# Kernel tuning notes

Measured on AMD Instinct MI355X. Metric: run time of the kernel, lower is better.

The kernel has to match this reference:

```python
import jax, jax.numpy as jnp
import numpy as np

B, S, C = 4, 4096, 1024   # batch, input_size (seq len), channels
H, D, DK = 16, 64, 256    # nhead, head dim, dim_k (Linformer projection)


def setup_inputs() -> dict:
    key = jax.random.key(0)
    ks = jax.random.split(key, 9)
    s_in = 1.0 / np.sqrt(C)
    s_e = 1.0 / np.sqrt(S)
    return {
        'x':   jax.random.normal(ks[0], (B, S, C), jnp.float32),
        # per-head Q/K/V projection weights (Linear(channels, dim, bias=False))
        'Wq':  jax.random.normal(ks[1], (H, D, C), jnp.float32) * s_in,
        'Wk':  jax.random.normal(ks[2], (H, D, C), jnp.float32) * s_in,
        'Wv':  jax.random.normal(ks[3], (H, D, C), jnp.float32) * s_in,
        # shared (layerwise) E/F Linear(input_size, dim_k) with bias
        'E_w': jax.random.normal(ks[4], (DK, S), jnp.float32) * s_e,
        'E_b': jnp.zeros((DK,), jnp.float32),
        'F_w': jax.random.normal(ks[5], (DK, S), jnp.float32) * s_e,
        'F_b': jnp.zeros((DK,), jnp.float32),
        # output projection Linear(dim*nhead, channels)
        'Wo':  jax.random.normal(ks[6], (C, H * D), jnp.float32) * (1.0 / np.sqrt(H * D)),
        'bo':  jnp.zeros((C,), jnp.float32),
    }


def reference(x, Wq, Wk, Wv, E_w, E_b, F_w, F_b, Wo, bo):
    b, s, c = x.shape
    h, d, _ = Wq.shape
    # per-head projections (vectorized over the Python head loop)
    Q = jnp.einsum('bsc,hdc->bhsd', x, Wq)            # [B,H,S,D]
    Kt = jnp.einsum('bsc,hdc->bhds', x, Wk)           # K already transposed: [B,H,D,S]
    Vt = jnp.einsum('bsc,hdc->bhds', x, Wv)           # [B,H,D,S]
    # Linformer low-rank projections along the sequence axis
    Kp = jnp.einsum('bhds,ks->bhdk', Kt, E_w) + E_b   # [B,H,D,DK]
    Vp = jnp.einsum('bhds,ks->bhdk', Vt, F_w) + F_b   # [B,H,D,DK]
    scores = jnp.einsum('bhsd,bhdk->bhsk', Q, Kp) / jnp.sqrt(jnp.asarray(d, x.dtype))
    P = jax.nn.softmax(scores, axis=-1)               # softmax over projected dim_k
    head_out = jnp.einsum('bhsk,bhdk->bhsd', P, Vp)   # [B,H,S,D]
    out = head_out.transpose(0, 2, 1, 3).reshape(b, s, h * d)  # concat heads
    return out @ Wo.T + bo
```

## Files before the change

### kernel.cpp

```cpp
#include <hip/hip_runtime.h>
#include <stdint.h>

typedef __attribute__((ext_vector_type(8))) short bf16x8;
typedef __attribute__((ext_vector_type(4))) float f32x4;
typedef __attribute__((ext_vector_type(16))) float f32x16;

__device__ __forceinline__ unsigned short f2b(float f) {
  union { float f; uint32_t u; } v; v.f = f;
  uint32_t u = v.u;
  return (unsigned short)((u + 0x7FFFu + ((u >> 16) & 1u)) >> 16);
}

__device__ __forceinline__ void gll16(const unsigned short* gsrc, unsigned short* lds_uniform) {
  __builtin_amdgcn_global_load_lds(
      (const __attribute__((address_space(1))) uint32_t*)gsrc,
      (__attribute__((address_space(3))) uint32_t*)lds_uniform,
      16, 0, 0);
}

#define MFMA(a, b, c) __builtin_amdgcn_mfma_f32_16x16x32_bf16((a), (b), (c), 0, 0, 0)
#define MFMA32(a, b, c) __builtin_amdgcn_mfma_f32_32x32x16_bf16((a), (b), (c), 0, 0, 0)

__global__ void cast_x_dual(const float* __restrict__ x,
                            unsigned short* __restrict__ xb,
                            unsigned short* __restrict__ xT) {
  __shared__ unsigned short tile[64][65];
  const int st = blockIdx.x * 64;
  const int ct = blockIdx.y * 64;
  const int b = blockIdx.z;
  const int t = threadIdx.x;
#pragma unroll
  for (int it = 0; it < 4; ++it) {
    int linear = (it * 256 + t) * 4;
    int r = linear >> 6, c = linear & 63;
    float4 v = *(const float4*)(x + ((size_t)(b * 4096 + st + r)) * 1024 + ct + c);
    ushort4 o;
    o.x = f2b(v.x); o.y = f2b(v.y); o.z = f2b(v.z); o.w = f2b(v.w);
    *(ushort4*)(xb + ((size_t)(b * 4096 + st + r)) * 1024 + ct + c) = o;
    tile[r][c] = o.x; tile[r][c + 1] = o.y; tile[r][c + 2] = o.z; tile[r][c + 3] = o.w;
  }
  __syncthreads();
#pragma unroll
  for (int it = 0; it < 4; ++it) {
    int linear = (it * 256 + t) * 4;
    int r = linear >> 6, c = linear & 63;
    ushort4 o;
    o.x = tile[c][r]; o.y = tile[c + 1][r]; o.z = tile[c + 2][r]; o.w = tile[c + 3][r];
    *(ushort4*)(xT + ((size_t)b * 1024 + ct + r) * 4096 + st + c) = o;
  }
}

__global__ void cast6(const float* __restrict__ s0, const float* __restrict__ s1,
                      const float* __restrict__ s2, const float* __restrict__ s3,
                      const float* __restrict__ s4, const float* __restrict__ s5,
                      const float* __restrict__ E_b, const float* __restrict__ F_b,
                      unsigned short* __restrict__ d0, unsigned short* __restrict__ d1,
                      unsigned short* __restrict__ d2, unsigned short* __restrict__ d3,
                      unsigned short* __restrict__ d4, unsigned short* __restrict__ d5,
                      float* __restrict__ EFbias) {
  if (blockIdx.y == 6) {
    if (blockIdx.x == 0) {
      int t = threadIdx.x;
      EFbias[t] = E_b[t];
      EFbias[256 + t] = F_b[t];
    }
    return;
  }
  const float* src; unsigned short* dst; float sc = 1.0f;
  switch (blockIdx.y) {
    case 0: src = s0; dst = d0; sc = 0.18033688011112042f; break;
    case 1: src = s1; dst = d1; break;
    case 2: src = s2; dst = d2; break;
    case 3: src = s3; dst = d3; break;
    case 4: src = s4; dst = d4; break;
    default: src = s5; dst = d5; break;
  }
  int i = (blockIdx.x * 256 + threadIdx.x) * 4;
  float4 v = *(const float4*)(src + i);
  ushort4 o;
  o.x = f2b(v.x * sc); o.y = f2b(v.y * sc); o.z = f2b(v.z * sc); o.w = f2b(v.w * sc);
  *(ushort4*)(dst + i) = o;
}

template <int BIAS, bool OBF16>
__global__ __launch_bounds__(512, 1) void gemm_bt256(
    const unsigned short* __restrict__ A, const unsigned short* __restrict__ B,
    void* __restrict__ Cout, const float* __restrict__ bias,
    int K, int lda, int ldb, int ldc) {
  __shared__ unsigned short Asm_[4][256 * 32];
  __shared__ unsigned short Bsm_[4][256 * 32];
  const int tid = threadIdx.x;
  const int wave = tid >> 6, lane = tid & 63;
  const int g = (lane >> 4) & 3, l15 = lane & 15;
  const int wmi = wave >> 2, wni = wave & 3;
  const int bm = blockIdx.x * 256, bn = blockIdx.y * 256;

  const int c0 = wave * 2;
  const int rr0 = c0 * 16 + (lane >> 2);
  const int rr1 = rr0 + 16;
  const int sl0 = (lane & 3) ^ ((rr0 >> 1) & 3);
  const int sl1 = (lane & 3) ^ ((rr1 >> 1) & 3);

#define STG(T, BUF)                                                                   \
  {                                                                                   \
    int kt_ = (T) * 32;                                                               \
    gll16(A + (size_t)(bm + rr0) * lda + kt_ + sl0 * 8, Asm_[BUF] + c0 * 512);        \
    gll16(B + (size_t)(bn + rr0) * ldb + kt_ + sl0 * 8, Bsm_[BUF] + c0 * 512);        \
    gll16(A + (size_t)(bm + rr1) * lda + kt_ + sl1 * 8, Asm_[BUF] + (c0 + 1) * 512);  \
    gll16(B + (size_t)(bn + rr1) * ldb + kt_ + sl1 * 8, Bsm_[BUF] + (c0 + 1) * 512);  \
  }

  f32x4 acc[8][4];
#pragma unroll
  for (int i = 0; i < 8; ++i)
#pragma unroll
    for (int j = 0; j < 4; ++j) acc[i][j] = (f32x4){0.f, 0.f, 0.f, 0.f};

  const int nt = K >> 5;
  STG(0, 0);
  if (nt > 1) STG(1, 1);
  if (nt > 2) STG(2, 2);
  asm volatile("s_waitcnt vmcnt(8)" ::: "memory");
  __builtin_amdgcn_s_barrier();
  asm volatile("" ::: "memory");

  for (int t = 0; t < nt; ++t) {
    const int cur = t & 3;
    const char* Ac = (const char*)Asm_[cur];
    const char* Bc = (const char*)Bsm_[cur];

    bf16x8 afr[8], bfr[4];
#pragma unroll
    for (int mf = 0; mf < 8; ++mf) {
      int m = wmi * 128 + mf * 16 + l15;
      afr[mf] = *(const bf16x8*)(Ac + m * 64 + ((g ^ ((m >> 1) & 3)) << 4));
    }
#pragma unroll
    for (int nf = 0; nf < 4; ++nf) {
      int n = wni * 64 + nf * 16 + l15;
      bfr[nf] = *(const bf16x8*)(Bc + n * 64 + ((g ^ ((n >> 1) & 3)) << 4));
    }

    if (t + 3 < nt) STG(t + 3, (t + 3) & 3);

    __builtin_amdgcn_s_setprio(1);
#pragma unroll
    for (int mf = 0; mf < 8; ++mf)
#pragma unroll
      for (int nf = 0; nf < 4; ++nf)
        acc[mf][nf] = MFMA(afr[mf], bfr[nf], acc[mf][nf]);
    __builtin_amdgcn_s_setprio(0);

    if (t + 3 < nt)      asm volatile("s_waitcnt vmcnt(8)" ::: "memory");
    else if (t + 2 < nt) asm volatile("s_waitcnt vmcnt(4)" ::: "memory");
    else                 asm volatile("s_waitcnt vmcnt(0)" ::: "memory");
    __builtin_amdgcn_s_barrier();
    asm volatile("" ::: "memory");
  }
#undef STG

#pragma unroll
  for (int mf = 0; mf < 8; ++mf)
#pragma unroll
    for (int r = 0; r < 4; ++r) {
      int row = bm + wmi * 128 + mf * 16 + g * 4 + r;
      float rb = (BIAS == 1) ? bias[row] : 0.f;
#pragma unroll
      for (int nf = 0; nf < 4; ++nf) {
        int col = bn + wni * 64 + nf * 16 + l15;
        float v = acc[mf][nf][r] + rb + ((BIAS == 2) ? bias[col] : 0.f);
        if (OBF16) ((unsigned short*)Cout)[(size_t)row * ldc + col] = f2b(v);
        else       ((float*)Cout)[(size_t)row * ldc + col] = v;
      }
    }
}

__global__ __launch_bounds__(256, 2) void gemm_xef_splitk(
    const unsigned short* __restrict__ A,
    const unsigned short* __restrict__ B,
    float* __restrict__ Cpart) {
  __shared__ unsigned short Asm_[2][128 * 32];
  __shared__ unsigned short Bsm_[2][128 * 32];
  const int tid = threadIdx.x;
  const int wave = tid >> 6, lane = tid & 63;
  const int g = lane >> 4, l15 = lane & 15;
  const int bm = blockIdx.x * 128, bn = blockIdx.y * 128;
  const int z = blockIdx.z, split = z >> 2, b = z & 3;
  const unsigned short* Ab = A + split * 1024;
  const unsigned short* Bb = B + (size_t)b * 1024 * 4096 + split * 1024;
  const int wm = (wave >> 1) * 64, wn = (wave & 1) * 64;

  const int rr0 = wave * 16 + (lane >> 2);
  const int rr1 = rr0 + 64;
  const int sl0 = (lane & 3) ^ ((rr0 >> 1) & 3);
  const int sl1 = (lane & 3) ^ ((rr1 >> 1) & 3);

#define XEF_STAGE(T, BUF)                                                           \
  {                                                                                 \
    int kt_ = (T) * 32;                                                             \
    gll16(Ab + (size_t)(bm + rr0) * 4096 + kt_ + sl0 * 8, Asm_[BUF] + wave * 512);  \
    gll16(Bb + (size_t)(bn + rr0) * 4096 + kt_ + sl0 * 8, Bsm_[BUF] + wave * 512);  \
    gll16(Ab + (size_t)(bm + rr1) * 4096 + kt_ + sl1 * 8, Asm_[BUF] + (wave + 4) * 512); \
    gll16(Bb + (size_t)(bn + rr1) * 4096 + kt_ + sl1 * 8, Bsm_[BUF] + (wave + 4) * 512); \
  }

  f32x4 acc[4][4];
#pragma unroll
  for (int i = 0; i < 4; ++i)
#pragma unroll
    for (int j = 0; j < 4; ++j) acc[i][j] = (f32x4){0.f, 0.f, 0.f, 0.f};

  const int nt = 32;
  XEF_STAGE(0, 0);
  for (int t = 0; t < nt; ++t) {
    const int cur = t & 1;
    if (t + 1 < nt) {
      XEF_STAGE(t + 1, cur ^ 1);
      asm volatile("s_waitcnt vmcnt(4)" ::: "memory");
    } else {
      asm volatile("s_waitcnt vmcnt(0)" ::: "memory");
    }
    __builtin_amdgcn_s_barrier();
    asm volatile("" ::: "memory");

    bf16x8 af[4], bfr[4];
    const char* Ac = (const char*)Asm_[cur];
    const char* Bc = (const char*)Bsm_[cur];
#pragma unroll
    for (int mi = 0; mi < 4; ++mi) {
      int m = wm + mi * 16 + l15;
      af[mi] = *(const bf16x8*)(Ac + m * 64 + ((g ^ ((m >> 1) & 3)) << 4));
    }
#pragma unroll
    for (int ni = 0; ni < 4; ++ni) {
      int n = wn + ni * 16 + l15;
      bfr[ni] = *(const bf16x8*)(Bc + n * 64 + ((g ^ ((n >> 1) & 3)) << 4));
    }
#pragma unroll
    for (int mi = 0; mi < 4; ++mi)
#pragma unroll
      for (int ni = 0; ni < 4; ++ni)
        acc[mi][ni] = MFMA(af[mi], bfr[ni], acc[mi][ni]);

    asm volatile("" ::: "memory");
    __builtin_amdgcn_s_barrier();
  }
#undef XEF_STAGE

  float* C = Cpart + (size_t)z * (512 * 1024);
#pragma unroll
  for (int mi = 0; mi < 4; ++mi)
#pragma unroll
    for (int r = 0; r < 4; ++r) {
      int row = bm + wm + mi * 16 + g * 4 + r;
#pragma unroll
      for (int ni = 0; ni < 4; ++ni) {
        int col = bn + wn + ni * 16 + l15;
        C[(size_t)row * 1024 + col] = acc[mi][ni][r];
      }
    }
}

__global__ void reduce_xef(const float* __restrict__ P,
                           const float* __restrict__ bias,
                           unsigned short* __restrict__ out) {
  int t = blockIdx.x * 256 + threadIdx.x;
  size_t flat = (size_t)t * 4;
  float4 s = *(const float4*)(P + flat);
#pragma unroll
  for (int sp = 1; sp < 4; ++sp) {
    float4 v = *(const float4*)(P + (size_t)sp * 2097152 + flat);
    s.x += v.x; s.y += v.y; s.z += v.z; s.w += v.w;
  }
  float rb = bias[(flat >> 10) & 511];
  ushort4 o;
  o.x = f2b(s.x + rb); o.y = f2b(s.y + rb);
  o.z = f2b(s.z + rb); o.w = f2b(s.w + rb);
  *(ushort4*)(out + flat) = o;
}

template <int BIAS, bool OBF16, int CMODE>
__global__ __launch_bounds__(256, 4) void gemm_bt64(
    const unsigned short* __restrict__ A, const unsigned short* __restrict__ B,
    void* __restrict__ Cout, const float* __restrict__ bias,
    int M, int N, int K, int lda, int ldb, int ldc,
    long long sA, long long sB, long long sC) {
  __shared__ unsigned short Asm_[2][64 * 32];
  __shared__ unsigned short Bsm_[2][64 * 32];
  const int tid = threadIdx.x;
  const int wave = tid >> 6, lane = tid & 63;
  const int g = lane >> 4, l15 = lane & 15;
  const int bm = blockIdx.x * 64, bn = blockIdx.y * 64;
  const unsigned short* Ab = A + (size_t)blockIdx.z * sA;
  const unsigned short* Bb = B + (size_t)blockIdx.z * sB;
  const int wm = (wave >> 1) * 32, wn = (wave & 1) * 32;

  const int rr = wave * 16 + (lane >> 2);
  const int sl = (lane & 3) ^ ((rr >> 1) & 3);

#define BT64_STAGE(T, BUF)                                                      \
  {                                                                             \
    int kt_ = (T) * 32;                                                         \
    gll16(Ab + (size_t)(bm + rr) * lda + kt_ + sl * 8, Asm_[BUF] + wave * 512); \
    gll16(Bb + (size_t)(bn + rr) * ldb + kt_ + sl * 8, Bsm_[BUF] + wave * 512); \
  }

  f32x4 acc[2][2];
#pragma unroll
  for (int i = 0; i < 2; ++i)
#pragma unroll
    for (int j = 0; j < 2; ++j) acc[i][j] = (f32x4){0.f, 0.f, 0.f, 0.f};

  const int nt = K >> 5;
  BT64_STAGE(0, 0);
  for (int t = 0; t < nt; ++t) {
    const int cur = t & 1;
    if (t + 1 < nt) {
      BT64_STAGE(t + 1, cur ^ 1);
      asm volatile("s_waitcnt vmcnt(2)" ::: "memory");
    } else {
      asm volatile("s_waitcnt vmcnt(0)" ::: "memory");
    }
    __builtin_amdgcn_s_barrier();
    asm volatile("" ::: "memory");

    bf16x8 af[2], bfr[2];
    const char* Ac = (const char*)Asm_[cur];
    const char* Bc = (const char*)Bsm_[cur];
#pragma unroll
    for (int mi = 0; mi < 2; ++mi) {
      int m = wm + mi * 16 + l15;
      af[mi] = *(const bf16x8*)(Ac + m * 64 + ((g ^ ((m >> 1) & 3)) << 4));
    }
#pragma unroll
    for (int ni = 0; ni < 2; ++ni) {
      int n = wn + ni * 16 + l15;
      bfr[ni] = *(const bf16x8*)(Bc + n * 64 + ((g ^ ((n >> 1) & 3)) << 4));
    }
#pragma unroll
    for (int mi = 0; mi < 2; ++mi)
#pragma unroll
      for (int ni = 0; ni < 2; ++ni)
        acc[mi][ni] = MFMA(af[mi], bfr[ni], acc[mi][ni]);

    asm volatile("" ::: "memory");
    __builtin_amdgcn_s_barrier();
  }
#undef BT64_STAGE

#pragma unroll
  for (int mi = 0; mi < 2; ++mi)
#pragma unroll
    for (int r = 0; r < 4; ++r) {
      int row = bm + wm + mi * 16 + g * 4 + r;
      float rb = (BIAS == 1) ? bias[row] : 0.f;
#pragma unroll
      for (int ni = 0; ni < 2; ++ni) {
        int col = bn + wn + ni * 16 + l15;
        float v = acc[mi][ni][r] + rb + ((BIAS == 2) ? bias[col] : 0.f);
        size_t idx;
        if (CMODE == 1) {
          idx = (size_t)(col >> 6) * ((size_t)M * 64) + (size_t)row * 64 + (col & 63);
        } else if (CMODE == 2) {
          int cl = col & 15;
          int cp = (cl & 3) | ((cl & 4) << 1) | ((cl & 8) >> 1);
          idx = (size_t)row * ldc + (col & ~15) + cp;
        } else {
          idx = (size_t)row * ldc + col;
        }
        if (OBF16) ((unsigned short*)Cout + (size_t)blockIdx.z * sC)[idx] = f2b(v);
        else       ((float*)Cout + (size_t)blockIdx.z * sC)[idx] = v;
      }
    }
}

__global__ __launch_bounds__(512, 2) void attn_kernel(
    const unsigned short* __restrict__ q,
    const unsigned short* __restrict__ kp,
    const unsigned short* __restrict__ vp,
    unsigned short* __restrict__ ho) {
  __shared__ unsigned short Ksm[256 * 64];
  __shared__ unsigned short Vsm[64 * 256];

  const int tid = threadIdx.x;
  const int wave = tid >> 6, lane = tid & 63;
  const int l31 = lane & 31, hi = lane >> 5;
  const int x = blockIdx.x;
  const int bh = (x & 7) + ((x >> 7) << 3);
  const int qq = (x >> 3) & 15;
  const int b = bh >> 4, h = bh & 15;
  const int s0 = qq * 256;

  const unsigned short* kph = kp + (size_t)bh * (256 * 64);
  const unsigned short* vph = vp + (size_t)bh * (64 * 256);

  {
    const int r = (lane >> 3), sl = (lane & 7) ^ (lane >> 3);
#pragma unroll
    for (int it = 0; it < 4; ++it) {
      int c = it * 8 + wave;
      gll16(kph + (c * 8 + r) * 64 + sl * 8, Ksm + c * 512);
    }
  }
  {
    const int rv = lane >> 5;
#pragma unroll
    for (int it = 0; it < 4; ++it) {
      int c = it * 8 + wave;
      int row = c * 2 + rv;
      int sl = (lane & 31) ^ (row & 7);
      gll16(vph + (size_t)row * 256 + sl * 8, Vsm + c * 512);
    }
  }

  const int srow = s0 + wave * 32 + l31;
  const unsigned short* qrow = q + (size_t)(b * 4096 + srow) * 1024 + h * 64;
  bf16x8 qf[4];
#pragma unroll
  for (int dc = 0; dc < 4; ++dc)
    qf[dc] = *(const bf16x8*)(qrow + dc * 16 + hi * 8);

  bf16x8 ones;
#pragma unroll
  for (int j = 0; j < 8; ++j) ones[j] = (short)0x3F80;

  __syncthreads();

  f32x16 ho0 = {0,0,0,0,0,0,0,0,0,0,0,0,0,0,0,0};
  f32x16 ho1 = {0,0,0,0,0,0,0,0,0,0,0,0,0,0,0,0};
  f32x16 sumacc = {0,0,0,0,0,0,0,0,0,0,0,0,0,0,0,0};

  const int vsw0 = l31 & 7;
#pragma unroll
  for (int t = 0; t < 8; ++t) {
    bf16x8 vf00 = *(const bf16x8*)((const char*)Vsm + l31 * 512 + (((t * 4 + hi) ^ vsw0) << 4));
    bf16x8 vf01 = *(const bf16x8*)((const char*)Vsm + l31 * 512 + (((t * 4 + 2 + hi) ^ vsw0) << 4));
    bf16x8 vf10 = *(const bf16x8*)((const char*)Vsm + (32 + l31) * 512 + (((t * 4 + hi) ^ vsw0) << 4));
    bf16x8 vf11 = *(const bf16x8*)((const char*)Vsm + (32 + l31) * 512 + (((t * 4 + 2 + hi) ^ vsw0) << 4));

    f32x16 qk = {0,0,0,0,0,0,0,0,0,0,0,0,0,0,0,0};
    const int krow = t * 32 + l31;
    const char* kbase = (const char*)Ksm + krow * 128;
#pragma unroll
    for (int dc = 0; dc < 4; ++dc) {
      bf16x8 kf = *(const bf16x8*)(kbase + (((dc * 2 + hi) ^ (l31 & 7)) << 4));
      qk = MFMA32(kf, qf[dc], qk);
    }

    uint32_t pk[8];
#pragma unroll
    for (int j = 0; j < 8; ++j) {
      float e0 = exp2f(qk[2 * j]);
      float e1 = exp2f(qk[2 * j + 1]);
      asm("v_cvt_pk_bf16_f32 %0, %1, %2" : "=v"(pk[j]) : "v"(e0), "v"(e1));
    }
    union { uint32_t u[4]; bf16x8 v; } ua, ub;
    ua.u[0] = pk[0]; ua.u[1] = pk[1]; ua.u[2] = pk[2]; ua.u[3] = pk[3];
    ub.u[0] = pk[4]; ub.u[1] = pk[5]; ub.u[2] = pk[6]; ub.u[3] = pk[7];

    ho0 = MFMA32(ua.v, vf00, ho0);
    ho0 = MFMA32(ub.v, vf01, ho0);
    ho1 = MFMA32(ua.v, vf10, ho1);
    ho1 = MFMA32(ub.v, vf11, ho1);
    sumacc = MFMA32(ua.v, ones, sumacc);
    sumacc = MFMA32(ub.v, ones, sumacc);
  }

  float rl[16];
#pragma unroll
  for (int reg = 0; reg < 16; ++reg)
    rl[reg] = __builtin_amdgcn_rcpf(sumacc[reg]);

  unsigned short* hob = ho + (size_t)(b * 4096 + s0 + wave * 32) * 1024 + h * 64 + l31;
#pragma unroll
  for (int reg = 0; reg < 16; ++reg) {
    int srw = (reg & 3) + 8 * (reg >> 2) + 4 * hi;
    hob[(size_t)srw * 1024]      = f2b(ho0[reg] * rl[reg]);
    hob[(size_t)srw * 1024 + 32] = f2b(ho1[reg] * rl[reg]);
  }
}

extern "C" void kernel_launch(void* const* d_in, const int* in_sizes, int n_in,
                              void* d_out, int out_size, void* d_ws, size_t ws_size,
                              hipStream_t stream) {
  (void)in_sizes; (void)n_in; (void)out_size; (void)ws_size;
  const float* x   = (const float*)d_in[0];
  const float* Wq  = (const float*)d_in[1];
  const float* Wk  = (const float*)d_in[2];
  const float* Wv  = (const float*)d_in[3];
  const float* E_w = (const float*)d_in[4];
  const float* E_b = (const float*)d_in[5];
  const float* F_w = (const float*)d_in[6];
  const float* F_b = (const float*)d_in[7];
  const float* Wo  = (const float*)d_in[8];
  const float* bo  = (const float*)d_in[9];
  float* out = (float*)d_out;

  char* ws = (char*)d_ws;
  unsigned short* xb   = (unsigned short*)(ws);
  unsigned short* xT   = (unsigned short*)(ws + 33554432);
  unsigned short* Qb   = (unsigned short*)(ws + 67108864);
  unsigned short* Wqb  = (unsigned short*)(ws + 100663296);
  unsigned short* Wkb  = (unsigned short*)(ws + 102760448);
  unsigned short* Wvb  = (unsigned short*)(ws + 104857600);
  unsigned short* Wob  = (unsigned short*)(ws + 106954752);
  unsigned short* EFb  = (unsigned short*)(ws + 109051904);
  unsigned short* xEF  = (unsigned short*)(ws + 113246208);
  unsigned short* Kp   = (unsigned short*)(ws + 117440512);
  unsigned short* Vp   = (unsigned short*)(ws + 119537664);
  float*          EFbias = (float*)(ws + 121634816);
  float*          Ppart  = (float*)(ws + 121700352);
  unsigned short* HO   = xb;

  cast_x_dual<<<dim3(64, 16, 4), 256, 0, stream>>>(x, xb, xT);
  cast6<<<dim3(1024, 7), 256, 0, stream>>>(
      Wq, Wk, Wv, E_w, F_w, Wo, E_b, F_b,
      Wqb, Wkb, Wvb, EFb, EFb + 2097152 / 2, Wob, EFbias);

  gemm_bt256<0, true><<<dim3(64, 4), 512, 0, stream>>>(
      xb, Wqb, Qb, nullptr, 1024, 1024, 1024, 1024);

  gemm_xef_splitk<<<dim3(4, 8, 16), 256, 0, stream>>>(EFb, xT, Ppart);
  reduce_xef<<<dim3(2048, 1, 1), 256, 0, stream>>>(Ppart, EFbias, xEF);

  gemm_bt64<0, true, 1><<<dim3(4, 16, 4), 256, 0, stream>>>(
      xEF, Wkb, Kp, nullptr, 256, 1024, 1024, 1024, 1024, 1024,
      512LL * 1024, 0LL, 256LL * 1024);

  gemm_bt64<0, true, 2><<<dim3(16, 4, 4), 256, 0, stream>>>(
      Wvb, xEF + 256 * 1024, Vp, nullptr, 1024, 256, 1024, 1024, 1024, 256,
      0LL, 512LL * 1024, 1024LL * 256);

  attn_kernel<<<dim3(1024, 1, 1), 512, 0, stream>>>(Qb, Kp, Vp, HO);

  gemm_bt256<2, false><<<dim3(64, 4), 512, 0, stream>>>(
      HO, Wob, out, bo, 1024, 1024, 1024, 1024);
}
```

Before: 206.5 us.

## Split GEMM main loop into two phases interleaving LDS reads, prefetch and MFMA

Restructures the gemm_bt256 inner loop into two half-iterations. Each half loads half of the A fragments, issues half of the global-to-LDS prefetch (A then B), and runs half of the MFMAs, with extra barriers between phases. The aim is to overlap LDS reads and global loads with matrix math and to lower register pressure from holding all eight A fragments at once. In exchange it adds more block-wide barriers per k-step, and the waitcnt accounting now depends on the split loads.

```diff
diff --git a/kernel.cpp b/kernel.cpp
--- a/kernel.cpp
+++ b/kernel.cpp
@@ -101,12 +101,16 @@
   const int sl0 = (lane & 3) ^ ((rr0 >> 1) & 3);
   const int sl1 = (lane & 3) ^ ((rr1 >> 1) & 3);
 
-#define STG(T, BUF)                                                                   \
+#define STGA(T, BUF)                                                                  \
   {                                                                                   \
     int kt_ = (T) * 32;                                                               \
     gll16(A + (size_t)(bm + rr0) * lda + kt_ + sl0 * 8, Asm_[BUF] + c0 * 512);        \
+    gll16(A + (size_t)(bm + rr1) * lda + kt_ + sl1 * 8, Asm_[BUF] + (c0 + 1) * 512);  \
+  }
+#define STGB(T, BUF)                                                                  \
+  {                                                                                   \
+    int kt_ = (T) * 32;                                                               \
     gll16(B + (size_t)(bn + rr0) * ldb + kt_ + sl0 * 8, Bsm_[BUF] + c0 * 512);        \
-    gll16(A + (size_t)(bm + rr1) * lda + kt_ + sl1 * 8, Asm_[BUF] + (c0 + 1) * 512);  \
     gll16(B + (size_t)(bn + rr1) * ldb + kt_ + sl1 * 8, Bsm_[BUF] + (c0 + 1) * 512);  \
   }
 
@@ -117,9 +121,9 @@
     for (int j = 0; j < 4; ++j) acc[i][j] = (f32x4){0.f, 0.f, 0.f, 0.f};
 
   const int nt = K >> 5;
-  STG(0, 0);
-  if (nt > 1) STG(1, 1);
-  if (nt > 2) STG(2, 2);
+  STGA(0, 0) STGB(0, 0)
+  if (nt > 1) { STGA(1, 1) STGB(1, 1) }
+  if (nt > 2) { STGA(2, 2) STGB(2, 2) }
   asm volatile("s_waitcnt vmcnt(8)" ::: "memory");
   __builtin_amdgcn_s_barrier();
   asm volatile("" ::: "memory");
@@ -128,36 +132,56 @@
     const int cur = t & 3;
     const char* Ac = (const char*)Asm_[cur];
     const char* Bc = (const char*)Bsm_[cur];
-
-    bf16x8 afr[8], bfr[4];
-#pragma unroll
-    for (int mf = 0; mf < 8; ++mf) {
-      int m = wmi * 128 + mf * 16 + l15;
-      afr[mf] = *(const bf16x8*)(Ac + m * 64 + ((g ^ ((m >> 1) & 3)) << 4));
-    }
+    const bool pf = (t + 3 < nt);
+    const int pbuf = (t + 3) & 3;
+
+    bf16x8 bfr[4], af0[4];
 #pragma unroll
     for (int nf = 0; nf < 4; ++nf) {
       int n = wni * 64 + nf * 16 + l15;
       bfr[nf] = *(const bf16x8*)(Bc + n * 64 + ((g ^ ((n >> 1) & 3)) << 4));
     }
-
-    if (t + 3 < nt) STG(t + 3, (t + 3) & 3);
-
+#pragma unroll
+    for (int mf = 0; mf < 4; ++mf) {
+      int m = wmi * 128 + mf * 16 + l15;
+      af0[mf] = *(const bf16x8*)(Ac + m * 64 + ((g ^ ((m >> 1) & 3)) << 4));
+    }
+    if (pf) STGA(t + 3, pbuf)
+    asm volatile("" ::: "memory");
+    __builtin_amdgcn_s_barrier();
     __builtin_amdgcn_s_setprio(1);
 #pragma unroll
-    for (int mf = 0; mf < 8; ++mf)
+    for (int mf = 0; mf < 4; ++mf)
 #pragma unroll
       for (int nf = 0; nf < 4; ++nf)
-        acc[mf][nf] = MFMA(afr[mf], bfr[nf], acc[mf][nf]);
+        acc[mf][nf] = MFMA(af0[mf], bfr[nf], acc[mf][nf]);
     __builtin_amdgcn_s_setprio(0);
-
-    if (t + 3 < nt)      asm volatile("s_waitcnt vmcnt(8)" ::: "memory");
+    asm volatile("" ::: "memory");
+    __builtin_amdgcn_s_barrier();
+
+    bf16x8 af1[4];
+#pragma unroll
+    for (int mf = 0; mf < 4; ++mf) {
+      int m = wmi * 128 + (4 + mf) * 16 + l15;
+      af1[mf] = *(const bf16x8*)(Ac + m * 64 + ((g ^ ((m >> 1) & 3)) << 4));
+    }
+    if (pf) STGB(t + 3, pbuf)
+    if (pf)              asm volatile("s_waitcnt vmcnt(8)" ::: "memory");
     else if (t + 2 < nt) asm volatile("s_waitcnt vmcnt(4)" ::: "memory");
     else                 asm volatile("s_waitcnt vmcnt(0)" ::: "memory");
     __builtin_amdgcn_s_barrier();
-    asm volatile("" ::: "memory");
-  }
-#undef STG
+    __builtin_amdgcn_s_setprio(1);
+#pragma unroll
+    for (int mf = 0; mf < 4; ++mf)
+#pragma unroll
+      for (int nf = 0; nf < 4; ++nf)
+        acc[4 + mf][nf] = MFMA(af1[mf], bfr[nf], acc[4 + mf][nf]);
+    __builtin_amdgcn_s_setprio(0);
+    asm volatile("" ::: "memory");
+    __builtin_amdgcn_s_barrier();
+  }
+#undef STGA
+#undef STGB
 
 #pragma unroll
   for (int mf = 0; mf < 8; ++mf)
```

New measurement: 209.1 us. About the same (+1.3%).
